# Performance work log

Hardware: AMD Instinct MI355X
Metric: run time of the kernel (lower is better)

Reference implementation:

```python
import jax, jax.numpy as jnp
import numpy as np

VOCAB, P, K, B, L, R = 50257, 512, 64, 32, 2048, 5


def setup_inputs() -> dict:
    key = jax.random.key(0)
    k1, k2, k3, k4, k5, k6, k7 = jax.random.split(key, 7)
    return {
        "x": jax.random.randint(k1, (B, L), 0, VOCAB, dtype=jnp.int32),
        "V": jax.random.normal(k2, (VOCAB, P), dtype=jnp.float32),
        "C": jax.random.normal(k3, (K, P), dtype=jnp.float32),
        "f1_w": jax.random.normal(k4, (2 * R + 1,), dtype=jnp.float32),
        "f1_b": jax.random.normal(k5, (K,), dtype=jnp.float32),
        "f2_w": jax.random.normal(k6, (K, P), dtype=jnp.float32),
        "f2_b": jax.random.normal(k7, (K,), dtype=jnp.float32),
    }


def reference(x, V, C, f1_w, f1_b, f2_w, f2_b):
    b, l = x.shape
    k, p = C.shape
    w = f1_w.shape[0]
    r = (w - 1) // 2
    emb = V[x]                                              # [B,L,P] embedding lookup
    x_hat = emb / jnp.linalg.norm(emb, axis=2, keepdims=True)
    l_hat = C / jnp.linalg.norm(C, axis=1, keepdims=True)
    G = jnp.einsum('kp,blp->bkl', l_hat, x_hat)             # cosine sim [B,K,L]
    # sliding-window dot product == depthwise 1D cross-correlation, 'same' padding
    u = jax.lax.conv_general_dilated(
        G.reshape(b * k, 1, l), f1_w.reshape(1, 1, w),
        window_strides=(1,), padding=[(r, r)],
        dimension_numbers=('NCH', 'OIH', 'NCH'),
    ).reshape(b, k, l)
    m = jax.nn.relu(u + f1_b[None, :, None])                # [B,K,L]
    beta = jax.nn.softmax(m.max(axis=1), axis=1)            # max over labels, softmax over seq -> [B,L]
    pooled = jnp.mean(beta[:, :, None] * emb, axis=1)       # [B,P]
    return pooled @ f2_w.T + f2_b                           # [B,K]
```

## Files before the change

kernel.cpp:

```cpp
#include <hip/hip_runtime.h>
#include <hip/hip_bf16.h>

#define PP     512
#define KK     64
#define BB     32
#define LLEN   2048
#define NPOS   (BB * LLEN)

typedef __attribute__((ext_vector_type(8)))  short short8;
typedef __attribute__((ext_vector_type(16))) float float16;

__device__ inline unsigned int pack_bf2(float lo, float hi) {
    __hip_bfloat162 h = __float22bfloat162_rn(make_float2(lo, hi));
    unsigned int u;
    __builtin_memcpy(&u, &h, 4);
    return u;
}
__device__ inline float bf_lo(unsigned int v) { return __uint_as_float(v << 16); }
__device__ inline float bf_hi(unsigned int v) { return __uint_as_float(v & 0xffff0000u); }

__global__ void k1_prep(const float* __restrict__ C, const float* __restrict__ f2w,
                        ushort* __restrict__ lhatB, ushort* __restrict__ f2wB) {
    const int n   = blockIdx.x & 63;
    const bool isW = blockIdx.x >= 64;
    const float* src = isW ? (f2w + n * PP) : (C + n * PP);
    ushort* dst = isW ? f2wB : lhatB;
    const int t = threadIdx.x;
    float v0 = src[t];
    float v1 = src[t + 256];
    __shared__ float red[256];
    red[t] = v0 * v0 + v1 * v1;
    __syncthreads();
    for (int s = 128; s > 0; s >>= 1) {
        if (t < s) red[t] += red[t + s];
        __syncthreads();
    }
    const float inv = isW ? 1.f : rsqrtf(red[0]);
    dst[(((t >> 3)      * 64 + n) << 3) + (t & 7)] = (ushort)(pack_bf2(v0 * inv, 0.f) & 0xffffu);
    dst[(((t >> 3) + 32) * 64 + n) * 8  + (t & 7)] = (ushort)(pack_bf2(v1 * inv, 0.f) & 0xffffu);
}

__launch_bounds__(256)
__global__ void k2_gemm(const int* __restrict__ x, const float* __restrict__ V,
                        const uint4* __restrict__ lhatB4, const uint4* __restrict__ f2wB4,
                        unsigned int* __restrict__ Gt2, unsigned int* __restrict__ E2p) {
    __shared__ uint4 sA[128 * 16];
    __shared__ uint4 sB[16 * 64];
    __shared__ uint4 sB2[16 * 64];
    __shared__ int   stok[128];
    __shared__ float rnorm[128];

    const int tid  = threadIdx.x;
    const int lane = tid & 63;
    const int wv   = tid >> 6;

    if (tid < 128) stok[tid] = x[blockIdx.x * 128 + tid];

    float16 acc0, acc1, acc2, acc3;
#pragma unroll
    for (int i = 0; i < 16; ++i) { acc0[i] = 0.f; acc1[i] = 0.f; acc2[i] = 0.f; acc3[i] = 0.f; }
    float nacc[8];
#pragma unroll
    for (int i = 0; i < 8; ++i) nacc[i] = 0.f;

    for (int kc = 0; kc < 4; ++kc) {
        __syncthreads();
#pragma unroll
        for (int i = 0; i < 8; ++i) {
            const int m = i * 16 + (tid >> 4);
            const int f = tid & 15;
            const float* src = V + (size_t)stok[m] * PP + kc * 128 + f * 8;
            const float4 a = ((const float4*)src)[0];
            const float4 b = ((const float4*)src)[1];
            uint4 wq;
            wq.x = pack_bf2(a.x, a.y); wq.y = pack_bf2(a.z, a.w);
            wq.z = pack_bf2(b.x, b.y); wq.w = pack_bf2(b.z, b.w);
            sA[m * 16 + (f ^ (m & 7))] = wq;
            float s2 = 0.f, e;
            e = bf_lo(wq.x); s2 = fmaf(e, e, s2);  e = bf_hi(wq.x); s2 = fmaf(e, e, s2);
            e = bf_lo(wq.y); s2 = fmaf(e, e, s2);  e = bf_hi(wq.y); s2 = fmaf(e, e, s2);
            e = bf_lo(wq.z); s2 = fmaf(e, e, s2);  e = bf_hi(wq.z); s2 = fmaf(e, e, s2);
            e = bf_lo(wq.w); s2 = fmaf(e, e, s2);  e = bf_hi(wq.w); s2 = fmaf(e, e, s2);
            nacc[i] += s2;
        }
#pragma unroll
        for (int i = 0; i < 4; ++i) {
            sB [i * 256 + tid] = lhatB4[kc * 1024 + i * 256 + tid];
            sB2[i * 256 + tid] = f2wB4 [kc * 1024 + i * 256 + tid];
        }

        if (kc == 3) {
#pragma unroll
            for (int i = 0; i < 8; ++i) {
                float r = nacc[i];
                r += __shfl_down(r, 8, 16);
                r += __shfl_down(r, 4, 16);
                r += __shfl_down(r, 2, 16);
                r += __shfl_down(r, 1, 16);
                if ((tid & 15) == 0) rnorm[i * 16 + (tid >> 4)] = rsqrtf(r);
            }
        }
        __syncthreads();

#pragma unroll
        for (int kb = 0; kb < 8; ++kb) {
            const int f  = kb * 2 + (lane >> 5);
            const int mq = wv * 32 + (lane & 31);
            const uint4 av = sA[mq * 16 + (f ^ (mq & 7))];
            const uint4 b0 = sB [f * 64 + (lane & 31)];
            const uint4 b1 = sB [f * 64 + 32 + (lane & 31)];
            const uint4 c0 = sB2[f * 64 + (lane & 31)];
            const uint4 c1 = sB2[f * 64 + 32 + (lane & 31)];
            short8 a8, t0, t1, t2, t3;
            __builtin_memcpy(&a8, &av, 16);
            __builtin_memcpy(&t0, &b0, 16);
            __builtin_memcpy(&t1, &b1, 16);
            __builtin_memcpy(&t2, &c0, 16);
            __builtin_memcpy(&t3, &c1, 16);
            acc0 = __builtin_amdgcn_mfma_f32_32x32x16_bf16(a8, t0, acc0, 0, 0, 0);
            acc1 = __builtin_amdgcn_mfma_f32_32x32x16_bf16(a8, t1, acc1, 0, 0, 0);
            acc2 = __builtin_amdgcn_mfma_f32_32x32x16_bf16(a8, t2, acc2, 0, 0, 0);
            acc3 = __builtin_amdgcn_mfma_f32_32x32x16_bf16(a8, t3, acc3, 0, 0, 0);
        }
    }

    const size_t posBase = (size_t)blockIdx.x * 128;
#pragma unroll
    for (int reg = 0; reg < 16; ++reg) {
        const int r  = (reg & 3) + 8 * (reg >> 2) + 4 * (lane >> 5);
        const int mq = wv * 32 + r;
        const float rn = rnorm[mq];
        const size_t p = posBase + mq;
        Gt2[p * 32 + (lane & 31)] = pack_bf2(acc0[reg] * rn, acc1[reg] * rn);
        E2p[p * 32 + (lane & 31)] = pack_bf2(acc2[reg], acc3[reg]);
    }
}

__global__ void k3_convmax(const unsigned int* __restrict__ Gt2, const float* __restrict__ f1w,
                           const float* __restrict__ f1b, float* __restrict__ mm) {
    __shared__ unsigned int sT[138 * 33];
    const int b  = blockIdx.x >> 4;
    const int l0 = (blockIdx.x & 15) * 128;
    const int t  = threadIdx.x;
    for (int idx = t; idx < 138 * 32; idx += 256) {
        const int row = idx >> 5, col = idx & 31;
        const int gl = l0 - 5 + row;
        sT[row * 33 + col] = (gl >= 0 && gl < LLEN)
            ? Gt2[((size_t)b * LLEN + gl) * 32 + col] : 0u;
    }
    __syncthreads();
    float w[11];
#pragma unroll
    for (int j = 0; j < 11; ++j) w[j] = f1w[j];
    const int j = t & 31;
    const int h = t >> 5;
    const float bias0 = f1b[j], bias1 = f1b[j + 32];
#pragma unroll 2
    for (int i = 0; i < 16; ++i) {
        const int lr = i * 8 + h;
        float u0 = 0.f, u1 = 0.f;
#pragma unroll
        for (int tap = 0; tap < 11; ++tap) {
            const unsigned int v = sT[(lr + tap) * 33 + j];
            u0 = fmaf(bf_lo(v), w[tap], u0);
            u1 = fmaf(bf_hi(v), w[tap], u1);
        }
        float m = fmaxf(fmaxf(u0 + bias0, 0.f), fmaxf(u1 + bias1, 0.f));
#pragma unroll
        for (int off = 16; off > 0; off >>= 1)
            m = fmaxf(m, __shfl_xor(m, off, 64));
        if (j == 0) mm[b * LLEN + l0 + lr] = m;
    }
}

__global__ void k4_softmax(const float* __restrict__ mm, float* __restrict__ beta) {
    const int b = blockIdx.x;
    const int t = threadIdx.x;
    __shared__ float red[256];
    float v[8];
    float mx = -1e30f;
#pragma unroll
    for (int i = 0; i < 8; ++i) {
        v[i] = mm[b * LLEN + t + i * 256];
        mx = fmaxf(mx, v[i]);
    }
    red[t] = mx;
    __syncthreads();
    for (int s = 128; s > 0; s >>= 1) {
        if (t < s) red[t] = fmaxf(red[t], red[t + s]);
        __syncthreads();
    }
    mx = red[0];
    __syncthreads();
    float sm = 0.f;
#pragma unroll
    for (int i = 0; i < 8; ++i) {
        v[i] = __expf(v[i] - mx);
        sm += v[i];
    }
    red[t] = sm;
    __syncthreads();
    for (int s = 128; s > 0; s >>= 1) {
        if (t < s) red[t] += red[t + s];
        __syncthreads();
    }
    const float inv = 1.f / red[0];
#pragma unroll
    for (int i = 0; i < 8; ++i) beta[b * LLEN + t + i * 256] = v[i] * inv;
}

__global__ void k5_pool(const unsigned int* __restrict__ E2p, const float* __restrict__ beta,
                        float* __restrict__ part2) {
    const int b = blockIdx.x >> 3;
    const int c = blockIdx.x & 7;
    const int t = threadIdx.x;
    const int j = t & 31, h = t >> 5;
    float a0 = 0.f, a1 = 0.f;
    const int lbase = c * 256;
#pragma unroll 4
    for (int i = 0; i < 32; ++i) {
        const int l = lbase + i * 8 + h;
        const float wgt = beta[b * LLEN + l];
        const unsigned int v = E2p[((size_t)b * LLEN + l) * 32 + j];
        a0 = fmaf(wgt, bf_lo(v), a0);
        a1 = fmaf(wgt, bf_hi(v), a1);
    }
    __shared__ float s[8][64];
    s[h][j]      = a0;
    s[h][j + 32] = a1;
    __syncthreads();
    if (t < 64) {
        float r = 0.f;
#pragma unroll
        for (int hh = 0; hh < 8; ++hh) r += s[hh][t];
        part2[blockIdx.x * 64 + t] = r;
    }
}

__global__ void k6_final(const float* __restrict__ part2, const float* __restrict__ f2b,
                         float* __restrict__ out) {
    const int o = blockIdx.x * 256 + threadIdx.x;
    const int k = o & 63;
    const int b = o >> 6;
    float r = 0.f;
#pragma unroll
    for (int c = 0; c < 8; ++c) r += part2[(b * 8 + c) * 64 + k];
    out[o] = r * (1.f / 2048.f) + f2b[k];
}

extern "C" void kernel_launch(void* const* d_in, const int* in_sizes, int n_in,
                              void* d_out, int out_size, void* d_ws, size_t ws_size,
                              hipStream_t stream) {
    const int*   x   = (const int*)d_in[0];
    const float* V   = (const float*)d_in[1];
    const float* C   = (const float*)d_in[2];
    const float* f1w = (const float*)d_in[3];
    const float* f1b = (const float*)d_in[4];
    const float* f2w = (const float*)d_in[5];
    const float* f2b = (const float*)d_in[6];
    float* out = (float*)d_out;

    float* ws = (float*)d_ws;
    ushort* lhatB = (ushort*)ws;
    ushort* f2wB  = (ushort*)(ws + 16384);
    unsigned int* Gt2 = (unsigned int*)(ws + 32768);
    unsigned int* E2p = Gt2 + (size_t)NPOS * 32;
    float* mm    = (float*)(E2p + (size_t)NPOS * 32);
    float* beta  = mm + NPOS;
    float* part2 = beta + NPOS;

    k1_prep   <<<128, 256, 0, stream>>>(C, f2w, lhatB, f2wB);
    k2_gemm   <<<NPOS / 128, 256, 0, stream>>>(x, V, (const uint4*)lhatB, (const uint4*)f2wB, Gt2, E2p);
    k3_convmax<<<BB * (LLEN / 128), 256, 0, stream>>>(Gt2, f1w, f1b, mm);
    k4_softmax<<<BB, 256, 0, stream>>>(mm, beta);
    k5_pool   <<<BB * 8, 256, 0, stream>>>(E2p, beta, part2);
    k6_final  <<<8, 256, 0, stream>>>(part2, f2b, out);
}
```

Measured before the change: 199.2 us.

## Halve GEMM M-tile, split waves across N, fuse softmax/pool/final kernels

The gather+MFMA kernel now processes 64 positions per block instead of 128. Its four waves split as 2 M-halves times 2 N-halves over a merged 128-column B matrix holding normalized C and f2w, which cuts accumulator registers and raises occupancy (launch bounds 256,3). The row norm is now computed from fp32 values rather than bf16-rounded ones. Softmax, pooling and the final bias are fused into one per-batch kernel, removing two launches and the beta/part2 round trips. The cost is that pooling runs on only 32 blocks, each streaming 2048 rows, which reduces parallelism in that stage.

```diff
diff --git a/kernel.cpp b/kernel.cpp
--- a/kernel.cpp
+++ b/kernel.cpp
@@ -20,11 +20,9 @@
 __device__ inline float bf_hi(unsigned int v) { return __uint_as_float(v & 0xffff0000u); }
 
 __global__ void k1_prep(const float* __restrict__ C, const float* __restrict__ f2w,
-                        ushort* __restrict__ lhatB, ushort* __restrict__ f2wB) {
-    const int n   = blockIdx.x & 63;
-    const bool isW = blockIdx.x >= 64;
-    const float* src = isW ? (f2w + n * PP) : (C + n * PP);
-    ushort* dst = isW ? f2wB : lhatB;
+                        ushort* __restrict__ Bu) {
+    const int n = blockIdx.x;
+    const float* src = (n < 64) ? (C + n * PP) : (f2w + (n - 64) * PP);
     const int t = threadIdx.x;
     float v0 = src[t];
     float v1 = src[t + 256];
@@ -35,39 +33,41 @@
         if (t < s) red[t] += red[t + s];
         __syncthreads();
     }
-    const float inv = isW ? 1.f : rsqrtf(red[0]);
-    dst[(((t >> 3)      * 64 + n) << 3) + (t & 7)] = (ushort)(pack_bf2(v0 * inv, 0.f) & 0xffffu);
-    dst[(((t >> 3) + 32) * 64 + n) * 8  + (t & 7)] = (ushort)(pack_bf2(v1 * inv, 0.f) & 0xffffu);
-}
-
-__launch_bounds__(256)
+    const float inv = (n < 64) ? rsqrtf(red[0]) : 1.f;
+    Bu[(((t >> 3)      * 128 + n) << 3) + (t & 7)] = (ushort)(pack_bf2(v0 * inv, 0.f) & 0xffffu);
+    Bu[((((t + 256) >> 3)) * 128 + n) * 8 + (t & 7)] = (ushort)(pack_bf2(v1 * inv, 0.f) & 0xffffu);
+}
+
+__launch_bounds__(256, 3)
 __global__ void k2_gemm(const int* __restrict__ x, const float* __restrict__ V,
-                        const uint4* __restrict__ lhatB4, const uint4* __restrict__ f2wB4,
+                        const uint4* __restrict__ Bu4,
                         unsigned int* __restrict__ Gt2, unsigned int* __restrict__ E2p) {
-    __shared__ uint4 sA[128 * 16];
-    __shared__ uint4 sB[16 * 64];
-    __shared__ uint4 sB2[16 * 64];
-    __shared__ int   stok[128];
-    __shared__ float rnorm[128];
+    __shared__ uint4 sA[64 * 16];
+    __shared__ uint4 sB[16 * 128];
+    __shared__ int   stok[64];
+    __shared__ float rnorm[64];
 
     const int tid  = threadIdx.x;
     const int lane = tid & 63;
     const int wv   = tid >> 6;
 
-    if (tid < 128) stok[tid] = x[blockIdx.x * 128 + tid];
-
-    float16 acc0, acc1, acc2, acc3;
-#pragma unroll
-    for (int i = 0; i < 16; ++i) { acc0[i] = 0.f; acc1[i] = 0.f; acc2[i] = 0.f; acc3[i] = 0.f; }
-    float nacc[8];
-#pragma unroll
-    for (int i = 0; i < 8; ++i) nacc[i] = 0.f;
+    if (tid < 64) stok[tid] = x[blockIdx.x * 64 + tid];
+
+    float16 acc0, acc1;
+#pragma unroll
+    for (int i = 0; i < 16; ++i) { acc0[i] = 0.f; acc1[i] = 0.f; }
+    float nacc[4];
+#pragma unroll
+    for (int i = 0; i < 4; ++i) nacc[i] = 0.f;
+
+    const int mt = (wv & 1) * 32;
+    const int nh = (wv >> 1) * 64;
 
     for (int kc = 0; kc < 4; ++kc) {
         __syncthreads();
 #pragma unroll
-        for (int i = 0; i < 8; ++i) {
-            const int m = i * 16 + (tid >> 4);
+        for (int i = 0; i < 4; ++i) {
+            const int m = (tid >> 4) + i * 16;
             const int f = tid & 15;
             const float* src = V + (size_t)stok[m] * PP + kc * 128 + f * 8;
             const float4 a = ((const float4*)src)[0];
@@ -76,28 +76,26 @@
             wq.x = pack_bf2(a.x, a.y); wq.y = pack_bf2(a.z, a.w);
             wq.z = pack_bf2(b.x, b.y); wq.w = pack_bf2(b.z, b.w);
             sA[m * 16 + (f ^ (m & 7))] = wq;
-            float s2 = 0.f, e;
-            e = bf_lo(wq.x); s2 = fmaf(e, e, s2);  e = bf_hi(wq.x); s2 = fmaf(e, e, s2);
-            e = bf_lo(wq.y); s2 = fmaf(e, e, s2);  e = bf_hi(wq.y); s2 = fmaf(e, e, s2);
-            e = bf_lo(wq.z); s2 = fmaf(e, e, s2);  e = bf_hi(wq.z); s2 = fmaf(e, e, s2);
-            e = bf_lo(wq.w); s2 = fmaf(e, e, s2);  e = bf_hi(wq.w); s2 = fmaf(e, e, s2);
+            float s2 = 0.f;
+            s2 = fmaf(a.x, a.x, s2); s2 = fmaf(a.y, a.y, s2);
+            s2 = fmaf(a.z, a.z, s2); s2 = fmaf(a.w, a.w, s2);
+            s2 = fmaf(b.x, b.x, s2); s2 = fmaf(b.y, b.y, s2);
+            s2 = fmaf(b.z, b.z, s2); s2 = fmaf(b.w, b.w, s2);
             nacc[i] += s2;
         }
 #pragma unroll
-        for (int i = 0; i < 4; ++i) {
-            sB [i * 256 + tid] = lhatB4[kc * 1024 + i * 256 + tid];
-            sB2[i * 256 + tid] = f2wB4 [kc * 1024 + i * 256 + tid];
-        }
+        for (int i = 0; i < 8; ++i)
+            sB[i * 256 + tid] = Bu4[kc * 2048 + i * 256 + tid];
 
         if (kc == 3) {
 #pragma unroll
-            for (int i = 0; i < 8; ++i) {
+            for (int i = 0; i < 4; ++i) {
                 float r = nacc[i];
                 r += __shfl_down(r, 8, 16);
                 r += __shfl_down(r, 4, 16);
                 r += __shfl_down(r, 2, 16);
                 r += __shfl_down(r, 1, 16);
-                if ((tid & 15) == 0) rnorm[i * 16 + (tid >> 4)] = rsqrtf(r);
+                if ((tid & 15) == 0) rnorm[(tid >> 4) + i * 16] = rsqrtf(r);
             }
         }
         __syncthreads();
@@ -105,34 +103,31 @@
 #pragma unroll
         for (int kb = 0; kb < 8; ++kb) {
             const int f  = kb * 2 + (lane >> 5);
-            const int mq = wv * 32 + (lane & 31);
+            const int mq = mt + (lane & 31);
             const uint4 av = sA[mq * 16 + (f ^ (mq & 7))];
-            const uint4 b0 = sB [f * 64 + (lane & 31)];
-            const uint4 b1 = sB [f * 64 + 32 + (lane & 31)];
-            const uint4 c0 = sB2[f * 64 + (lane & 31)];
-            const uint4 c1 = sB2[f * 64 + 32 + (lane & 31)];
-            short8 a8, t0, t1, t2, t3;
+            const uint4 b0 = sB[f * 128 + nh + (lane & 31)];
+            const uint4 b1 = sB[f * 128 + nh + 32 + (lane & 31)];
+            short8 a8, t0, t1;
             __builtin_memcpy(&a8, &av, 16);
             __builtin_memcpy(&t0, &b0, 16);
             __builtin_memcpy(&t1, &b1, 16);
-            __builtin_memcpy(&t2, &c0, 16);
-            __builtin_memcpy(&t3, &c1, 16);
             acc0 = __builtin_amdgcn_mfma_f32_32x32x16_bf16(a8, t0, acc0, 0, 0, 0);
             acc1 = __builtin_amdgcn_mfma_f32_32x32x16_bf16(a8, t1, acc1, 0, 0, 0);
-            acc2 = __builtin_amdgcn_mfma_f32_32x32x16_bf16(a8, t2, acc2, 0, 0, 0);
-            acc3 = __builtin_amdgcn_mfma_f32_32x32x16_bf16(a8, t3, acc3, 0, 0, 0);
-        }
-    }
-
-    const size_t posBase = (size_t)blockIdx.x * 128;
+        }
+    }
+
+    const size_t posBase = (size_t)blockIdx.x * 64;
 #pragma unroll
     for (int reg = 0; reg < 16; ++reg) {
         const int r  = (reg & 3) + 8 * (reg >> 2) + 4 * (lane >> 5);
-        const int mq = wv * 32 + r;
-        const float rn = rnorm[mq];
+        const int mq = mt + r;
         const size_t p = posBase + mq;
-        Gt2[p * 32 + (lane & 31)] = pack_bf2(acc0[reg] * rn, acc1[reg] * rn);
-        E2p[p * 32 + (lane & 31)] = pack_bf2(acc2[reg], acc3[reg]);
+        if (wv < 2) {
+            const float rn = rnorm[mq];
+            Gt2[p * 32 + (lane & 31)] = pack_bf2(acc0[reg] * rn, acc1[reg] * rn);
+        } else {
+            E2p[p * 32 + (lane & 31)] = pack_bf2(acc0[reg], acc1[reg]);
+        }
     }
 }
 
@@ -173,10 +168,14 @@
     }
 }
 
-__global__ void k4_softmax(const float* __restrict__ mm, float* __restrict__ beta) {
+__global__ void k7_softpool(const float* __restrict__ mm, const unsigned int* __restrict__ E2p,
+                            const float* __restrict__ f2b, float* __restrict__ out) {
     const int b = blockIdx.x;
     const int t = threadIdx.x;
     __shared__ float red[256];
+    __shared__ float sbeta[LLEN];
+    __shared__ float sred[8][64];
+
     float v[8];
     float mx = -1e30f;
 #pragma unroll
@@ -206,46 +205,28 @@
     }
     const float inv = 1.f / red[0];
 #pragma unroll
-    for (int i = 0; i < 8; ++i) beta[b * LLEN + t + i * 256] = v[i] * inv;
-}
-
-__global__ void k5_pool(const unsigned int* __restrict__ E2p, const float* __restrict__ beta,
-                        float* __restrict__ part2) {
-    const int b = blockIdx.x >> 3;
-    const int c = blockIdx.x & 7;
-    const int t = threadIdx.x;
+    for (int i = 0; i < 8; ++i) sbeta[t + i * 256] = v[i] * inv;
+    __syncthreads();
+
     const int j = t & 31, h = t >> 5;
     float a0 = 0.f, a1 = 0.f;
-    const int lbase = c * 256;
-#pragma unroll 4
-    for (int i = 0; i < 32; ++i) {
-        const int l = lbase + i * 8 + h;
-        const float wgt = beta[b * LLEN + l];
-        const unsigned int v = E2p[((size_t)b * LLEN + l) * 32 + j];
-        a0 = fmaf(wgt, bf_lo(v), a0);
-        a1 = fmaf(wgt, bf_hi(v), a1);
-    }
-    __shared__ float s[8][64];
-    s[h][j]      = a0;
-    s[h][j + 32] = a1;
+#pragma unroll 8
+    for (int i = 0; i < 256; ++i) {
+        const int l = i * 8 + h;
+        const float wgt = sbeta[l];
+        const unsigned int e = E2p[((size_t)b * LLEN + l) * 32 + j];
+        a0 = fmaf(wgt, bf_lo(e), a0);
+        a1 = fmaf(wgt, bf_hi(e), a1);
+    }
+    sred[h][j]      = a0;
+    sred[h][j + 32] = a1;
     __syncthreads();
     if (t < 64) {
         float r = 0.f;
 #pragma unroll
-        for (int hh = 0; hh < 8; ++hh) r += s[hh][t];
-        part2[blockIdx.x * 64 + t] = r;
-    }
-}
-
-__global__ void k6_final(const float* __restrict__ part2, const float* __restrict__ f2b,
-                         float* __restrict__ out) {
-    const int o = blockIdx.x * 256 + threadIdx.x;
-    const int k = o & 63;
-    const int b = o >> 6;
-    float r = 0.f;
-#pragma unroll
-    for (int c = 0; c < 8; ++c) r += part2[(b * 8 + c) * 64 + k];
-    out[o] = r * (1.f / 2048.f) + f2b[k];
+        for (int hh = 0; hh < 8; ++hh) r += sred[hh][t];
+        out[b * KK + t] = r * (1.f / 2048.f) + f2b[t];
+    }
 }
 
 extern "C" void kernel_launch(void* const* d_in, const int* in_sizes, int n_in,
@@ -261,18 +242,13 @@
     float* out = (float*)d_out;
 
     float* ws = (float*)d_ws;
-    ushort* lhatB = (ushort*)ws;
-    ushort* f2wB  = (ushort*)(ws + 16384);
+    ushort* Bu = (ushort*)ws;
     unsigned int* Gt2 = (unsigned int*)(ws + 32768);
     unsigned int* E2p = Gt2 + (size_t)NPOS * 32;
-    float* mm    = (float*)(E2p + (size_t)NPOS * 32);
-    float* beta  = mm + NPOS;
-    float* part2 = beta + NPOS;
-
-    k1_prep   <<<128, 256, 0, stream>>>(C, f2w, lhatB, f2wB);
-    k2_gemm   <<<NPOS / 128, 256, 0, stream>>>(x, V, (const uint4*)lhatB, (const uint4*)f2wB, Gt2, E2p);
-    k3_convmax<<<BB * (LLEN / 128), 256, 0, stream>>>(Gt2, f1w, f1b, mm);
-    k4_softmax<<<BB, 256, 0, stream>>>(mm, beta);
-    k5_pool   <<<BB * 8, 256, 0, stream>>>(E2p, beta, part2);
-    k6_final  <<<8, 256, 0, stream>>>(part2, f2b, out);
-}
+    float* mm = (float*)(E2p + (size_t)NPOS * 32);
+
+    k1_prep    <<<128, 256, 0, stream>>>(C, f2w, Bu);
+    k2_gemm    <<<NPOS / 64, 256, 0, stream>>>(x, V, (const uint4*)Bu, Gt2, E2p);
+    k3_convmax <<<BB * (LLEN / 128), 256, 0, stream>>>(Gt2, f1w, f1b, mm);
+    k7_softpool<<<BB, 256, 0, stream>>>(mm, E2p, f2b, out);
+}
```

New measurement: 200.6 us. No clear change (+0.7%).
